# Kernel tuning notes

Hardware: AMD Instinct MI355X
Metric: run time of the kernel (lower is better)

Reference implementation:

```python
import jax, jax.numpy as jnp
import numpy as np

N, E, S = 10000, 100000, 10            # nodes, edges, message-passing steps
NODE_F, EDGE_F, L, H, OUT = 30, 4, 128, 128, 3


def _mlp(h, W0, b0, W1, b1, W2, b2):
    # Linear->ReLU, Linear->ReLU, Linear (build_mlp with num_hidden_layers=2)
    h = jax.nn.relu(h @ W0 + b0)
    h = jax.nn.relu(h @ W1 + b1)
    return h @ W2 + b2


def _ln(h, g, b):
    # torch.nn.LayerNorm over last dim, eps=1e-5, biased variance
    m = h.mean(-1, keepdims=True)
    v = h.var(-1, keepdims=True)
    return (h - m) * jax.lax.rsqrt(v + 1e-5) * g + b


def setup_inputs():
    key = jax.random.key(0)
    ks = iter(jax.random.split(key, 64))

    def w(shape, fan):
        return jax.random.normal(next(ks), shape, dtype=jnp.float32) / np.float32(np.sqrt(fan))

    d = {}
    d["x"] = jax.random.normal(next(ks), (N, NODE_F), dtype=jnp.float32)
    d["ea"] = jax.random.normal(next(ks), (E, EDGE_F), dtype=jnp.float32)
    d["ei"] = jax.random.randint(next(ks), (2, E), 0, N)
    # encoder node ('en') / edge ('ee') MLP+LayerNorm params
    for pre, fin in (("en", NODE_F), ("ee", EDGE_F)):
        d[pre + "W0"] = w((fin, H), fin); d[pre + "b0"] = jnp.zeros((H,), jnp.float32)
        d[pre + "W1"] = w((H, H), H);     d[pre + "b1"] = jnp.zeros((H,), jnp.float32)
        d[pre + "W2"] = w((H, L), H);     d[pre + "b2"] = jnp.zeros((L,), jnp.float32)
        d[pre + "g"] = jnp.ones((L,), jnp.float32); d[pre + "bt"] = jnp.zeros((L,), jnp.float32)
    # processor edge ('pe', in=3L) / node ('pn', in=2L) params, stacked over S steps
    for pre, fin in (("pe", 3 * L), ("pn", 2 * L)):
        d[pre + "W0"] = w((S, fin, H), fin); d[pre + "b0"] = jnp.zeros((S, H), jnp.float32)
        d[pre + "W1"] = w((S, H, H), H);     d[pre + "b1"] = jnp.zeros((S, H), jnp.float32)
        d[pre + "W2"] = w((S, H, L), H);     d[pre + "b2"] = jnp.zeros((S, L), jnp.float32)
        d[pre + "g"] = jnp.ones((S, L), jnp.float32); d[pre + "bt"] = jnp.zeros((S, L), jnp.float32)
    # decoder MLP (no LayerNorm)
    d["dW0"] = w((L, H), L); d["db0"] = jnp.zeros((H,), jnp.float32)
    d["dW1"] = w((H, H), H); d["db1"] = jnp.zeros((H,), jnp.float32)
    d["dW2"] = w((H, OUT), H); d["db2"] = jnp.zeros((OUT,), jnp.float32)
    return d


def reference(x, ea, ei,
              enW0, enb0, enW1, enb1, enW2, enb2, eng, enbt,
              eeW0, eeb0, eeW1, eeb1, eeW2, eeb2, eeg, eebt,
              peW0, peb0, peW1, peb1, peW2, peb2, peg, pebt,
              pnW0, pnb0, pnW1, pnb1, pnW2, pnb2, png, pnbt,
              dW0, db0, dW1, db1, dW2, db2):
    src, dst = ei[0], ei[1]
    # encode (GraphIndependent)
    hx = _ln(_mlp(x, enW0, enb0, enW1, enb1, enW2, enb2), eng, enbt)   # [N, L]
    he = _ln(_mlp(ea, eeW0, eeb0, eeW1, eeb1, eeW2, eeb2), eeg, eebt)  # [E, L]

    # process: S InteractionNetwork steps with residuals
    def step(carry, p):
        cx, ce = carry
        (eW0, eb0, eW1, eb1, eW2, eb2, eg, ebt,
         nW0, nb0, nW1, nb1, nW2, nb2, ng, nbt) = p
        edge_in = jnp.concatenate([cx[src], cx[dst], ce], axis=-1)     # [E, 3L]
        ue = _ln(_mlp(edge_in, eW0, eb0, eW1, eb1, eW2, eb2), eg, ebt)  # [E, L]
        agg = jax.ops.segment_sum(ue, dst, num_segments=N)              # [N, L]
        un = _ln(_mlp(jnp.concatenate([cx, agg], axis=-1), nW0, nb0, nW1, nb1, nW2, nb2), ng, nbt)
        return (cx + un, ce + ue), None

    (hx, he), _ = jax.lax.scan(
        step, (hx, he),
        (peW0, peb0, peW1, peb1, peW2, peb2, peg, pebt,
         pnW0, pnb0, pnW1, pnb1, pnW2, pnb2, png, pnbt))

    # decode
    return _mlp(hx, dW0, db0, dW1, db1, dW2, db2)  # [N, OUT]
```

## Files before the change

### kernel.cpp

```cpp
#include <hip/hip_runtime.h>


#define NN 10000
#define NE 100000
#define STEPS 10
#define NODE_F 30
#define EDGE_F 4
#define L 128
#define AP 132
#define BP 36

#define WS_STRIDE 136
#define AB_STRIDE 136

typedef __bf16 bf16x8 __attribute__((ext_vector_type(8)));
typedef float f32x4 __attribute__((ext_vector_type(4)));

__device__ __forceinline__ unsigned short f2bf(float f) {
  __bf16 b = (__bf16)f;
  return __builtin_bit_cast(unsigned short, b);
}
__device__ __forceinline__ float bf2f(unsigned short u) {
  return __builtin_bit_cast(float, (unsigned)u << 16);
}


__device__ __forceinline__ void stage_W(unsigned short* __restrict__ Ws,
                                        const unsigned short* __restrict__ Wt,
                                        int K, int sec, int tid) {
#pragma unroll
  for (int p = 0; p < 8; ++p) {
    int u = tid + p * 256;
    int n = u >> 4, kk = u & 15;
    uint4 v = *(const uint4*)(Wt + (size_t)n * K + sec * 128 + kk * 8);
    *(uint4*)&Ws[n * WS_STRIDE + kk * 8] = v;
  }
}


__device__ __forceinline__ void init_acc(f32x4 acc[2][4], const float* __restrict__ b,
                                         int wcol, int l16) {
#pragma unroll
  for (int j = 0; j < 4; ++j) {
    float bv = b[wcol + j * 16 + l16];
#pragma unroll
    for (int i = 0; i < 2; ++i) acc[i][j] = f32x4{bv, bv, bv, bv};
  }
}

__device__ __forceinline__ void layer_gbf(const unsigned short* __restrict__ ap0,
                                          const unsigned short* __restrict__ ap1,
                                          const unsigned short* __restrict__ Ws,
                                          f32x4 acc[2][4], int wcol, int l4, int l16) {
#pragma unroll
  for (int kk = 0; kk < 4; ++kk) {
    bf16x8 af[2];
    af[0] = *(const bf16x8*)(ap0 + kk * 32 + l4 * 8);
    af[1] = *(const bf16x8*)(ap1 + kk * 32 + l4 * 8);
#pragma unroll
    for (int j = 0; j < 4; ++j) {
      bf16x8 bv = *(const bf16x8*)&Ws[(wcol + j * 16 + l16) * WS_STRIDE + kk * 32 + l4 * 8];
#pragma unroll
      for (int i = 0; i < 2; ++i)
        acc[i][j] = __builtin_amdgcn_mfma_f32_16x16x32_bf16(af[i], bv, acc[i][j], 0, 0, 0);
    }
  }
}

__device__ __forceinline__ void layer_lds(const unsigned short* __restrict__ Ab,
                                          const unsigned short* __restrict__ Ws,
                                          f32x4 acc[2][4], int wrow, int wcol, int l4, int l16) {
#pragma unroll
  for (int kk = 0; kk < 4; ++kk) {
    bf16x8 af[2];
#pragma unroll
    for (int i = 0; i < 2; ++i)
      af[i] = *(const bf16x8*)&Ab[(wrow + i * 16 + l16) * AB_STRIDE + kk * 32 + l4 * 8];
#pragma unroll
    for (int j = 0; j < 4; ++j) {
      bf16x8 bv = *(const bf16x8*)&Ws[(wcol + j * 16 + l16) * WS_STRIDE + kk * 32 + l4 * 8];
#pragma unroll
      for (int i = 0; i < 2; ++i)
        acc[i][j] = __builtin_amdgcn_mfma_f32_16x16x32_bf16(af[i], bv, acc[i][j], 0, 0, 0);
    }
  }
}

__device__ __forceinline__ void relu_to_Ab(unsigned short* __restrict__ Ab, f32x4 acc[2][4],
                                           int wrow, int wcol, int l4, int l16) {
#pragma unroll
  for (int i = 0; i < 2; ++i)
#pragma unroll
    for (int j = 0; j < 4; ++j)
#pragma unroll
      for (int r = 0; r < 4; ++r) {
        int row = wrow + i * 16 + l4 * 4 + r;
        int col = wcol + j * 16 + l16;
        Ab[row * AB_STRIDE + col] = f2bf(fmaxf(acc[i][j][r], 0.f));
      }
}

__device__ __forceinline__ void ln_partials(const f32x4 acc[2][4], float ps[2][4], float ps2[2][4]) {
#pragma unroll
  for (int i = 0; i < 2; ++i)
#pragma unroll
    for (int r = 0; r < 4; ++r) {
      float s = 0.f, s2 = 0.f;
#pragma unroll
      for (int j = 0; j < 4; ++j) { float v = acc[i][j][r]; s += v; s2 += v * v; }
#pragma unroll
      for (int off = 1; off < 16; off <<= 1) {
        s += __shfl_xor(s, off, 64);
        s2 += __shfl_xor(s2, off, 64);
      }
      ps[i][r] = s; ps2[i][r] = s2;
    }
}


__global__ __launch_bounds__(256) void deg_kernel(const int* __restrict__ ei, int* __restrict__ cnt) {
  int e = blockIdx.x * 256 + threadIdx.x;
  if (e < NE) atomicAdd(&cnt[ei[NE + e]], 1);
}

__global__ __launch_bounds__(256) void scan_kernel(const int* __restrict__ cnt,
                                                   int* __restrict__ off, int* __restrict__ cur) {
  __shared__ int sums[256];
  int t = threadIdx.x;
  int base = t * 40;
  int local = 0;
  for (int i = 0; i < 40; ++i) { int n = base + i; if (n < NN) local += cnt[n]; }
  sums[t] = local;
  __syncthreads();
  int val = local;
  for (int d = 1; d < 256; d <<= 1) {
    int add = (t >= d) ? sums[t - d] : 0;
    __syncthreads();
    sums[t] += add;
    __syncthreads();
  }
  int run = sums[t] - val;
  for (int i = 0; i < 40; ++i) {
    int n = base + i;
    if (n < NN) { off[n] = run; cur[n] = run; run += cnt[n]; }
  }
  if (t == 255) off[NN] = sums[255];
}

__global__ __launch_bounds__(256) void scatter_kernel(const int* __restrict__ ei,
                                                      int* __restrict__ cur, int* __restrict__ eid) {
  int e = blockIdx.x * 256 + threadIdx.x;
  if (e < NE) { int p = atomicAdd(&cur[ei[NE + e]], 1); eid[p] = e; }
}


__global__ __launch_bounds__(256) void edge_step_mfma(
    const unsigned short* __restrict__ hx_bf, unsigned short* __restrict__ he_bf,
    unsigned short* __restrict__ ue_bf,
    const int* __restrict__ ei,
    const unsigned short* __restrict__ W0t, const float* __restrict__ b0,
    const unsigned short* __restrict__ W1t, const float* __restrict__ b1,
    const unsigned short* __restrict__ W2t, const float* __restrict__ b2,
    const float* __restrict__ g, const float* __restrict__ bt) {
  __shared__ __align__(16) unsigned short Ws[128 * WS_STRIDE];
  __shared__ __align__(16) unsigned short Ab[64 * AB_STRIDE];
  __shared__ int sidx[64], didx[64];
  int tid = threadIdx.x;
  int w = tid >> 6, lane = tid & 63;
  int l4 = lane >> 4, l16 = lane & 15;
  int wrow = (w >> 1) * 32, wcol = (w & 1) * 64;
  int e0 = blockIdx.x * 64;
  if (tid < 64) {
    int e = min(e0 + tid, NE - 1);
    sidx[tid] = ei[e];
    didx[tid] = ei[NE + e];
  }
  f32x4 acc[2][4];
  init_acc(acc, b0, wcol, l16);
  __syncthreads();
  for (int sec = 0; sec < 3; ++sec) {
    stage_W(Ws, W0t, 384, sec, tid);
    const unsigned short* ap[2];
#pragma unroll
    for (int i = 0; i < 2; ++i) {
      int r = wrow + i * 16 + l16;
      if (sec == 0)      ap[i] = hx_bf + (size_t)sidx[r] * L;
      else if (sec == 1) ap[i] = hx_bf + (size_t)didx[r] * L;
      else               ap[i] = he_bf + (size_t)min(e0 + r, NE - 1) * L;
    }
    __syncthreads();
    layer_gbf(ap[0], ap[1], Ws, acc, wcol, l4, l16);
    __syncthreads();
  }
  relu_to_Ab(Ab, acc, wrow, wcol, l4, l16);
  stage_W(Ws, W1t, 128, 0, tid);
  init_acc(acc, b1, wcol, l16);
  __syncthreads();
  layer_lds(Ab, Ws, acc, wrow, wcol, l4, l16);
  __syncthreads();
  relu_to_Ab(Ab, acc, wrow, wcol, l4, l16);
  stage_W(Ws, W2t, 128, 0, tid);
  init_acc(acc, b2, wcol, l16);
  __syncthreads();
  layer_lds(Ab, Ws, acc, wrow, wcol, l4, l16);
  float ps[2][4], ps2[2][4];
  ln_partials(acc, ps, ps2);
  __syncthreads();
  float* red = (float*)Ab;
  if (l16 == 0) {
#pragma unroll
    for (int i = 0; i < 2; ++i)
#pragma unroll
      for (int r = 0; r < 4; ++r) {
        int row = wrow + i * 16 + l4 * 4 + r;
        red[(w & 1) * 128 + row * 2 + 0] = ps[i][r];
        red[(w & 1) * 128 + row * 2 + 1] = ps2[i][r];
      }
  }
  __syncthreads();
  float gv[4], btv[4];
#pragma unroll
  for (int j = 0; j < 4; ++j) {
    int col = wcol + j * 16 + l16;
    gv[j] = g[col]; btv[j] = bt[col];
  }
#pragma unroll
  for (int i = 0; i < 2; ++i)
#pragma unroll
    for (int r = 0; r < 4; ++r) {
      int row = wrow + i * 16 + l4 * 4 + r;
      float s  = red[row * 2]     + red[128 + row * 2];
      float s2 = red[row * 2 + 1] + red[128 + row * 2 + 1];
      float m = s * (1.f / 128.f);
      float inv = rsqrtf(s2 * (1.f / 128.f) - m * m + 1e-5f);
      int e = e0 + row;
      if (e < NE) {
        size_t hoff = (size_t)e * L;
#pragma unroll
        for (int j = 0; j < 4; ++j) {
          int col = wcol + j * 16 + l16;
          float u = (acc[i][j][r] - m) * inv * gv[j] + btv[j];
          unsigned short old = he_bf[hoff + col];
          he_bf[hoff + col] = f2bf(bf2f(old) + u);
          ue_bf[hoff + col] = f2bf(u);
        }
      }
    }
}


__global__ __launch_bounds__(256) void node_step_mfma(
    float* __restrict__ hx, unsigned short* __restrict__ hx_bf,
    const unsigned short* __restrict__ ue_bf,
    const int* __restrict__ off, const int* __restrict__ eid,
    const unsigned short* __restrict__ W0t, const float* __restrict__ b0,
    const unsigned short* __restrict__ W1t, const float* __restrict__ b1,
    const unsigned short* __restrict__ W2t, const float* __restrict__ b2,
    const float* __restrict__ g, const float* __restrict__ bt) {
  __shared__ __align__(16) unsigned short Ws[128 * WS_STRIDE];
  __shared__ __align__(16) unsigned short Ab[64 * AB_STRIDE];
  __shared__ __align__(16) unsigned short Ag[64 * AB_STRIDE];
  int tid = threadIdx.x;
  int w = tid >> 6, lane = tid & 63;
  int l4 = lane >> 4, l16 = lane & 15;
  int wrow = (w >> 1) * 32, wcol = (w & 1) * 64;
  int n0 = blockIdx.x * 64;
  {
    int r = tid >> 2;
    int cseg = (tid & 3) * 32;
    int n = n0 + r;
    float a[32];
#pragma unroll
    for (int q = 0; q < 32; ++q) a[q] = 0.f;
    if (n < NN) {
      int p0 = off[n], p1 = off[n + 1];
      for (int p = p0; p < p1; ++p) {
        const unsigned short* row = ue_bf + (size_t)eid[p] * L + cseg;
#pragma unroll
        for (int q = 0; q < 4; ++q) {
          uint4 v = *(const uint4*)(row + q * 8);
          a[q * 8 + 0] += __builtin_bit_cast(float, v.x << 16);
          a[q * 8 + 1] += __builtin_bit_cast(float, v.x & 0xffff0000u);
          a[q * 8 + 2] += __builtin_bit_cast(float, v.y << 16);
          a[q * 8 + 3] += __builtin_bit_cast(float, v.y & 0xffff0000u);
          a[q * 8 + 4] += __builtin_bit_cast(float, v.z << 16);
          a[q * 8 + 5] += __builtin_bit_cast(float, v.z & 0xffff0000u);
          a[q * 8 + 6] += __builtin_bit_cast(float, v.w << 16);
          a[q * 8 + 7] += __builtin_bit_cast(float, v.w & 0xffff0000u);
        }
      }
    }
#pragma unroll
    for (int q = 0; q < 16; ++q) {
      unsigned o = (unsigned)f2bf(a[2 * q]) | ((unsigned)f2bf(a[2 * q + 1]) << 16);
      *(unsigned*)&Ag[r * AB_STRIDE + cseg + 2 * q] = o;
    }
  }
  stage_W(Ws, W0t, 256, 0, tid);
  f32x4 acc[2][4];
  init_acc(acc, b0, wcol, l16);
  __syncthreads();
  {
    const unsigned short* ap[2];
#pragma unroll
    for (int i = 0; i < 2; ++i)
      ap[i] = hx_bf + (size_t)min(n0 + wrow + i * 16 + l16, NN - 1) * L;
    layer_gbf(ap[0], ap[1], Ws, acc, wcol, l4, l16);
  }
  __syncthreads();
  stage_W(Ws, W0t, 256, 1, tid);
  __syncthreads();
  layer_lds(Ag, Ws, acc, wrow, wcol, l4, l16);
  __syncthreads();
  relu_to_Ab(Ab, acc, wrow, wcol, l4, l16);
  stage_W(Ws, W1t, 128, 0, tid);
  init_acc(acc, b1, wcol, l16);
  __syncthreads();
  layer_lds(Ab, Ws, acc, wrow, wcol, l4, l16);
  __syncthreads();
  relu_to_Ab(Ab, acc, wrow, wcol, l4, l16);
  stage_W(Ws, W2t, 128, 0, tid);
  init_acc(acc, b2, wcol, l16);
  __syncthreads();
  layer_lds(Ab, Ws, acc, wrow, wcol, l4, l16);
  float ps[2][4], ps2[2][4];
  ln_partials(acc, ps, ps2);
  __syncthreads();
  float* red = (float*)Ab;
  if (l16 == 0) {
#pragma unroll
    for (int i = 0; i < 2; ++i)
#pragma unroll
      for (int r = 0; r < 4; ++r) {
        int row = wrow + i * 16 + l4 * 4 + r;
        red[(w & 1) * 128 + row * 2 + 0] = ps[i][r];
        red[(w & 1) * 128 + row * 2 + 1] = ps2[i][r];
      }
  }
  __syncthreads();
  float gv[4], btv[4];
#pragma unroll
  for (int j = 0; j < 4; ++j) {
    int col = wcol + j * 16 + l16;
    gv[j] = g[col]; btv[j] = bt[col];
  }
#pragma unroll
  for (int i = 0; i < 2; ++i)
#pragma unroll
    for (int r = 0; r < 4; ++r) {
      int row = wrow + i * 16 + l4 * 4 + r;
      float s  = red[row * 2]     + red[128 + row * 2];
      float s2 = red[row * 2 + 1] + red[128 + row * 2 + 1];
      float m = s * (1.f / 128.f);
      float inv = rsqrtf(s2 * (1.f / 128.f) - m * m + 1e-5f);
      int n = n0 + row;
      if (n < NN) {
#pragma unroll
        for (int j = 0; j < 4; ++j) {
          int col = wcol + j * 16 + l16;
          float un = (acc[i][j][r] - m) * inv * gv[j] + btv[j];
          float nv = hx[(size_t)n * L + col] + un;
          hx[(size_t)n * L + col] = nv;
          hx_bf[(size_t)n * L + col] = f2bf(nv);
        }
      }
    }
}


__global__ __launch_bounds__(256) void enc_edge_mfma(
    const float* __restrict__ ea,
    const float* __restrict__ W0, const float* __restrict__ b0,
    const unsigned short* __restrict__ W1t, const float* __restrict__ b1,
    const unsigned short* __restrict__ W2t, const float* __restrict__ b2,
    const float* __restrict__ g, const float* __restrict__ bt,
    unsigned short* __restrict__ he_bf) {
  __shared__ __align__(16) unsigned short Ws[128 * WS_STRIDE];
  __shared__ __align__(16) unsigned short Ab[64 * AB_STRIDE];
  int tid = threadIdx.x;
  int w = tid >> 6, lane = tid & 63;
  int l4 = lane >> 4, l16 = lane & 15;
  int wrow = (w >> 1) * 32, wcol = (w & 1) * 64;
  int e0 = blockIdx.x * 64;
  {
    int row = tid >> 2, cbase = (tid & 3) * 32;
    int e = min(e0 + row, NE - 1);
    float4 eav = *(const float4*)&ea[(size_t)e * 4];
#pragma unroll
    for (int c = 0; c < 32; ++c) {
      int col = cbase + c;
      float sum = b0[col] + eav.x * W0[col] + eav.y * W0[128 + col] +
                  eav.z * W0[256 + col] + eav.w * W0[384 + col];
      Ab[row * AB_STRIDE + col] = f2bf(fmaxf(sum, 0.f));
    }
  }
  stage_W(Ws, W1t, 128, 0, tid);
  f32x4 acc[2][4];
  init_acc(acc, b1, wcol, l16);
  __syncthreads();
  layer_lds(Ab, Ws, acc, wrow, wcol, l4, l16);
  __syncthreads();
  relu_to_Ab(Ab, acc, wrow, wcol, l4, l16);
  stage_W(Ws, W2t, 128, 0, tid);
  init_acc(acc, b2, wcol, l16);
  __syncthreads();
  layer_lds(Ab, Ws, acc, wrow, wcol, l4, l16);
  float ps[2][4], ps2[2][4];
  ln_partials(acc, ps, ps2);
  __syncthreads();
  float* red = (float*)Ab;
  if (l16 == 0) {
#pragma unroll
    for (int i = 0; i < 2; ++i)
#pragma unroll
      for (int r = 0; r < 4; ++r) {
        int row = wrow + i * 16 + l4 * 4 + r;
        red[(w & 1) * 128 + row * 2 + 0] = ps[i][r];
        red[(w & 1) * 128 + row * 2 + 1] = ps2[i][r];
      }
  }
  __syncthreads();
  float gv[4], btv[4];
#pragma unroll
  for (int j = 0; j < 4; ++j) {
    int col = wcol + j * 16 + l16;
    gv[j] = g[col]; btv[j] = bt[col];
  }
#pragma unroll
  for (int i = 0; i < 2; ++i)
#pragma unroll
    for (int r = 0; r < 4; ++r) {
      int row = wrow + i * 16 + l4 * 4 + r;
      float s  = red[row * 2]     + red[128 + row * 2];
      float s2 = red[row * 2 + 1] + red[128 + row * 2 + 1];
      float m = s * (1.f / 128.f);
      float inv = rsqrtf(s2 * (1.f / 128.f) - m * m + 1e-5f);
      int e = e0 + row;
      if (e < NE) {
#pragma unroll
        for (int j = 0; j < 4; ++j) {
          int col = wcol + j * 16 + l16;
          he_bf[(size_t)e * L + col] = f2bf((acc[i][j][r] - m) * inv * gv[j] + btv[j]);
        }
      }
    }
}


__global__ __launch_bounds__(256) void wprep_kernel(
    const float* __restrict__ W0, const float* __restrict__ W1, const float* __restrict__ W2,
    unsigned short* __restrict__ out, int K0, int steps) {
  int per_step = 128 * (K0 + 256);
  int idx = blockIdx.x * 256 + threadIdx.x;
  if (idx >= steps * per_step) return;
  int s = idx / per_step, r = idx - s * per_step;
  float v;
  if (r < 128 * K0) {
    int n = r / K0, k = r - n * K0;
    v = W0[(size_t)s * K0 * 128 + (size_t)k * 128 + n];
  } else {
    r -= 128 * K0;
    const float* W = (r < 16384) ? W1 : W2;
    r &= 16383;
    int n = r >> 7, k = r & 127;
    v = W[(size_t)s * 16384 + k * 128 + n];
  }
  out[idx] = f2bf(v);
}

__global__ __launch_bounds__(256) void tprep_kernel(
    const float* __restrict__ W1, const float* __restrict__ W2, unsigned short* __restrict__ out) {
  int idx = blockIdx.x * 256 + threadIdx.x;
  const float* W = (idx < 16384) ? W1 : W2;
  int r = idx & 16383;
  int n = r >> 7, k = r & 127;
  out[idx] = f2bf(W[k * 128 + n]);
}


__device__ __forceinline__ void load_B(float* __restrict__ Bs, const float* __restrict__ W,
                                       int K, int k0, int tid) {
#pragma unroll
  for (int p = 0; p < 16; ++p) {
    int idx = tid + p * 256;
    int kk = idx >> 7;
    int c = idx & 127;
    float v = 0.f;
    if (k0 + kk < K) v = W[(size_t)(k0 + kk) * L + c];
    Bs[c * BP + kk] = v;
  }
}

__device__ __forceinline__ void fma32(const float* __restrict__ As, const float* __restrict__ Bs,
                                      float acc[4][8], int ty, int tx, int koff) {
#pragma unroll
  for (int kk = 0; kk < 32; kk += 4) {
    float4 a[4];
    float4 b[8];
#pragma unroll
    for (int i = 0; i < 4; ++i)
      a[i] = *(const float4*)&As[(ty + 16 * i) * AP + koff + kk];
#pragma unroll
    for (int j = 0; j < 8; ++j)
      b[j] = *(const float4*)&Bs[(tx + 16 * j) * BP + kk];
#pragma unroll
    for (int i = 0; i < 4; ++i)
#pragma unroll
      for (int j = 0; j < 8; ++j) {
        acc[i][j] = fmaf(a[i].x, b[j].x, acc[i][j]);
        acc[i][j] = fmaf(a[i].y, b[j].y, acc[i][j]);
        acc[i][j] = fmaf(a[i].z, b[j].z, acc[i][j]);
        acc[i][j] = fmaf(a[i].w, b[j].w, acc[i][j]);
      }
  }
}

__device__ __forceinline__ void init_bias(float acc[4][8], const float* __restrict__ b, int tx) {
#pragma unroll
  for (int j = 0; j < 8; ++j) {
    float bv = b[tx + 16 * j];
#pragma unroll
    for (int i = 0; i < 4; ++i) acc[i][j] = bv;
  }
}

__device__ __forceinline__ void store_relu(float* __restrict__ As, float acc[4][8], int ty, int tx) {
#pragma unroll
  for (int i = 0; i < 4; ++i)
#pragma unroll
    for (int j = 0; j < 8; ++j)
      As[(ty + 16 * i) * AP + tx + 16 * j] = fmaxf(acc[i][j], 0.f);
}

__device__ __forceinline__ void layer_As(const float* __restrict__ As, float* __restrict__ Bs,
                                         const float* __restrict__ W, const float* __restrict__ bias,
                                         int K, float acc[4][8], int tid, int ty, int tx) {
  init_bias(acc, bias, tx);
  int nc = (K + 31) >> 5;
  for (int bc = 0; bc < nc; ++bc) {
    __syncthreads();
    load_B(Bs, W, K, bc * 32, tid);
    __syncthreads();
    fma32(As, Bs, acc, ty, tx, bc * 32);
  }
}

__device__ __forceinline__ void fillA_gather(float* __restrict__ As, const float* __restrict__ base,
                                             const int* __restrict__ ridx, int tid) {
#pragma unroll
  for (int p = 0; p < 8; ++p) {
    int idx = tid + p * 256;
    int r = idx >> 5;
    int c4 = idx & 31;
    float4 v = *(const float4*)&base[(size_t)ridx[r] * L + c4 * 4];
    *(float4*)&As[r * AP + c4 * 4] = v;
  }
}

__device__ __forceinline__ void lnorm(float acc[4][8], const float* __restrict__ g,
                                      const float* __restrict__ bt, int tx) {
  float gv[8], bv[8];
#pragma unroll
  for (int j = 0; j < 8; ++j) { gv[j] = g[tx + 16 * j]; bv[j] = bt[tx + 16 * j]; }
#pragma unroll
  for (int i = 0; i < 4; ++i) {
    float s = 0.f, s2 = 0.f;
#pragma unroll
    for (int j = 0; j < 8; ++j) { s += acc[i][j]; s2 += acc[i][j] * acc[i][j]; }
#pragma unroll
    for (int off = 1; off < 16; off <<= 1) {
      s  += __shfl_xor(s, off, 64);
      s2 += __shfl_xor(s2, off, 64);
    }
    float m = s * (1.f / 128.f);
    float var = s2 * (1.f / 128.f) - m * m;
    float inv = rsqrtf(var + 1e-5f);
#pragma unroll
    for (int j = 0; j < 8; ++j) acc[i][j] = (acc[i][j] - m) * inv * gv[j] + bv[j];
  }
}

__global__ __launch_bounds__(256) void enc_node_kernel(
    const float* __restrict__ x,
    const float* __restrict__ W0, const float* __restrict__ b0,
    const float* __restrict__ W1, const float* __restrict__ b1,
    const float* __restrict__ W2, const float* __restrict__ b2,
    const float* __restrict__ g, const float* __restrict__ bt,
    float* __restrict__ hx, unsigned short* __restrict__ hx_bf) {
  __shared__ float As[64 * AP];
  __shared__ float Bs[128 * BP];
  int tid = threadIdx.x, ty = tid >> 4, tx = tid & 15;
  int n0 = blockIdx.x * 64;
#pragma unroll
  for (int p = 0; p < 8; ++p) {
    int idx = tid + p * 256;
    int r = idx >> 5, c = idx & 31;
    int n = min(n0 + r, NN - 1);
    As[r * AP + c] = (c < NODE_F) ? x[(size_t)n * NODE_F + c] : 0.f;
  }
  float acc[4][8];
  init_bias(acc, b0, tx);
  __syncthreads();
  load_B(Bs, W0, NODE_F, 0, tid);
  __syncthreads();
  fma32(As, Bs, acc, ty, tx, 0);

  __syncthreads(); store_relu(As, acc, ty, tx);
  layer_As(As, Bs, W1, b1, L, acc, tid, ty, tx);
  __syncthreads(); store_relu(As, acc, ty, tx);
  layer_As(As, Bs, W2, b2, L, acc, tid, ty, tx);
  lnorm(acc, g, bt, tx);
#pragma unroll
  for (int i = 0; i < 4; ++i) {
    int n = n0 + ty + 16 * i;
    if (n < NN)
#pragma unroll
      for (int j = 0; j < 8; ++j) {
        float v = acc[i][j];
        hx[(size_t)n * L + tx + 16 * j] = v;
        hx_bf[(size_t)n * L + tx + 16 * j] = f2bf(v);
      }
  }
}

__global__ __launch_bounds__(256) void dec_kernel(
    const float* __restrict__ hx,
    const float* __restrict__ W0, const float* __restrict__ b0,
    const float* __restrict__ W1, const float* __restrict__ b1,
    const float* __restrict__ W2, const float* __restrict__ b2,
    float* __restrict__ out) {
  __shared__ float As[64 * AP];
  __shared__ float Bs[128 * BP];
  __shared__ int nidx[64];
  int tid = threadIdx.x, ty = tid >> 4, tx = tid & 15;
  int n0 = blockIdx.x * 64;
  if (tid < 64) nidx[tid] = min(n0 + tid, NN - 1);
  __syncthreads();
  fillA_gather(As, hx, nidx, tid);
  float acc[4][8];
  layer_As(As, Bs, W0, b0, L, acc, tid, ty, tx);
  __syncthreads(); store_relu(As, acc, ty, tx);
  layer_As(As, Bs, W1, b1, L, acc, tid, ty, tx);
  __syncthreads(); store_relu(As, acc, ty, tx);
  __syncthreads();
  if (tid < 192) {
    int r = tid / 3, o = tid - (tid / 3) * 3;
    int n = n0 + r;
    if (n < NN) {
      float s = b2[o];
#pragma unroll 8
      for (int k = 0; k < L; ++k) s = fmaf(As[r * AP + k], W2[k * 3 + o], s);
      out[(size_t)n * 3 + o] = s;
    }
  }
}


extern "C" void kernel_launch(void* const* d_in, const int* in_sizes, int n_in,
                              void* d_out, int out_size, void* d_ws, size_t ws_size,
                              hipStream_t stream) {
  (void)in_sizes; (void)n_in; (void)out_size; (void)ws_size;
  const float* x    = (const float*)d_in[0];
  const float* ea   = (const float*)d_in[1];
  const int*   ei   = (const int*)d_in[2];
  const float* enW0 = (const float*)d_in[3];  const float* enb0 = (const float*)d_in[4];
  const float* enW1 = (const float*)d_in[5];  const float* enb1 = (const float*)d_in[6];
  const float* enW2 = (const float*)d_in[7];  const float* enb2 = (const float*)d_in[8];
  const float* eng  = (const float*)d_in[9];  const float* enbt = (const float*)d_in[10];
  const float* eeW0 = (const float*)d_in[11]; const float* eeb0 = (const float*)d_in[12];
  const float* eeW1 = (const float*)d_in[13]; const float* eeb1 = (const float*)d_in[14];
  const float* eeW2 = (const float*)d_in[15]; const float* eeb2 = (const float*)d_in[16];
  const float* eeg  = (const float*)d_in[17]; const float* eebt = (const float*)d_in[18];
  const float* peW0 = (const float*)d_in[19]; const float* peb0 = (const float*)d_in[20];
  const float* peW1 = (const float*)d_in[21]; const float* peb1 = (const float*)d_in[22];
  const float* peW2 = (const float*)d_in[23]; const float* peb2 = (const float*)d_in[24];
  const float* peg  = (const float*)d_in[25]; const float* pebt = (const float*)d_in[26];
  const float* pnW0 = (const float*)d_in[27]; const float* pnb0 = (const float*)d_in[28];
  const float* pnW1 = (const float*)d_in[29]; const float* pnb1 = (const float*)d_in[30];
  const float* pnW2 = (const float*)d_in[31]; const float* pnb2 = (const float*)d_in[32];
  const float* png  = (const float*)d_in[33]; const float* pnbt = (const float*)d_in[34];
  const float* dW0  = (const float*)d_in[35]; const float* db0  = (const float*)d_in[36];
  const float* dW1  = (const float*)d_in[37]; const float* db1  = (const float*)d_in[38];
  const float* dW2  = (const float*)d_in[39]; const float* db2  = (const float*)d_in[40];

  const size_t F_HX = (size_t)NN * L, F_HE = (size_t)NE * L;
  const size_t W_PE = 819200, W_PN = 655360, W_EE = 32768;

  float* hx = (float*)d_ws;
  unsigned short* he_bf  = (unsigned short*)(hx + F_HX);
  unsigned short* ue_bf  = he_bf + F_HE;
  unsigned short* hx_bf  = ue_bf + F_HE;
  unsigned short* wt_pe  = hx_bf + F_HX;
  unsigned short* wt_pn  = wt_pe + W_PE;
  unsigned short* wt_ee  = wt_pn + W_PN;
  int* cnt = (int*)(wt_ee + W_EE);
  int* off = cnt + NN;
  int* cur = off + NN + 1;
  int* eid = cur + NN;

  dim3 blk(256);
  int grid_n = (NN + 63) / 64;
  int grid_e = (NE + 63) / 64;

  wprep_kernel<<<(10 * 81920 + 255) / 256, blk, 0, stream>>>(peW0, peW1, peW2, wt_pe, 384, 10);
  wprep_kernel<<<(10 * 65536 + 255) / 256, blk, 0, stream>>>(pnW0, pnW1, pnW2, wt_pn, 256, 10);
  tprep_kernel<<<128, blk, 0, stream>>>(eeW1, eeW2, wt_ee);

  hipMemsetAsync(cnt, 0, (size_t)NN * 4, stream);
  deg_kernel<<<(NE + 255) / 256, blk, 0, stream>>>(ei, cnt);
  scan_kernel<<<1, blk, 0, stream>>>(cnt, off, cur);
  scatter_kernel<<<(NE + 255) / 256, blk, 0, stream>>>(ei, cur, eid);

  enc_node_kernel<<<grid_n, blk, 0, stream>>>(x, enW0, enb0, enW1, enb1, enW2, enb2, eng, enbt, hx, hx_bf);
  enc_edge_mfma<<<grid_e, blk, 0, stream>>>(ea, eeW0, eeb0, wt_ee, eeb1, wt_ee + 16384, eeb2, eeg, eebt, he_bf);

  for (int s = 0; s < STEPS; ++s) {
    const unsigned short* pe = wt_pe + (size_t)s * 81920;
    const unsigned short* pn = wt_pn + (size_t)s * 65536;
    edge_step_mfma<<<grid_e, blk, 0, stream>>>(
        hx_bf, he_bf, ue_bf, ei,
        pe,                 peb0 + (size_t)s * L,
        pe + 49152,         peb1 + (size_t)s * L,
        pe + 49152 + 16384, peb2 + (size_t)s * L,
        peg + (size_t)s * L, pebt + (size_t)s * L);
    node_step_mfma<<<grid_n, blk, 0, stream>>>(
        hx, hx_bf, ue_bf, off, eid,
        pn,                 pnb0 + (size_t)s * L,
        pn + 32768,         pnb1 + (size_t)s * L,
        pn + 32768 + 16384, pnb2 + (size_t)s * L,
        png + (size_t)s * L, pnbt + (size_t)s * L);
  }

  dec_kernel<<<grid_n, blk, 0, stream>>>(hx, dW0, db0, dW1, db1, dW2, db2, (float*)d_out);
}
```

Measured before the change: 947.7 us.

## Process 128 edges per block in edge step to amortize weight staging

The edge-step kernel now handles two 64-edge sub-tiles per block with two accumulator sets. Each staged weight tile in LDS is reused for both sub-tiles, which halves weight staging traffic and block count. Bias, gamma and beta loads are hoisted into registers, and the LayerNorm reduction scratch moves to the Ws buffer. The cost is higher register pressure from doubled accumulators, which may lower occupancy, plus more serialized syncs inside each block.

After: 1.353 ms. 1.43x slower.

```diff
diff --git a/kernel.cpp b/kernel.cpp
--- a/kernel.cpp
+++ b/kernel.cpp
@@ -45,6 +45,15 @@
     float bv = b[wcol + j * 16 + l16];
 #pragma unroll
     for (int i = 0; i < 2; ++i) acc[i][j] = f32x4{bv, bv, bv, bv};
+  }
+}
+
+__device__ __forceinline__ void init_acc_v(f32x4 acc[2][4], const float bv[4]) {
+#pragma unroll
+  for (int j = 0; j < 4; ++j) {
+    f32x4 b = {bv[j], bv[j], bv[j], bv[j]};
+#pragma unroll
+    for (int i = 0; i < 2; ++i) acc[i][j] = b;
   }
 }
 
@@ -164,85 +173,128 @@
     const float* __restrict__ g, const float* __restrict__ bt) {
   __shared__ __align__(16) unsigned short Ws[128 * WS_STRIDE];
   __shared__ __align__(16) unsigned short Ab[64 * AB_STRIDE];
-  __shared__ int sidx[64], didx[64];
+  __shared__ int sidx[128], didx[128];
   int tid = threadIdx.x;
   int w = tid >> 6, lane = tid & 63;
   int l4 = lane >> 4, l16 = lane & 15;
   int wrow = (w >> 1) * 32, wcol = (w & 1) * 64;
-  int e0 = blockIdx.x * 64;
-  if (tid < 64) {
+  int e0 = blockIdx.x * 128;
+  if (tid < 128) {
     int e = min(e0 + tid, NE - 1);
     sidx[tid] = ei[e];
     didx[tid] = ei[NE + e];
   }
-  f32x4 acc[2][4];
-  init_acc(acc, b0, wcol, l16);
+  float bv0[4], bv1[4], bv2[4], gv[4], btv[4];
+#pragma unroll
+  for (int j = 0; j < 4; ++j) {
+    int c = wcol + j * 16 + l16;
+    bv0[j] = b0[c]; bv1[j] = b1[c]; bv2[j] = b2[c]; gv[j] = g[c]; btv[j] = bt[c];
+  }
+  f32x4 acc0[2][4], acc1[2][4];
+  init_acc_v(acc0, bv0);
+  init_acc_v(acc1, bv0);
   __syncthreads();
   for (int sec = 0; sec < 3; ++sec) {
     stage_W(Ws, W0t, 384, sec, tid);
-    const unsigned short* ap[2];
+    const unsigned short* a0[2];
+    const unsigned short* a1[2];
 #pragma unroll
     for (int i = 0; i < 2; ++i) {
       int r = wrow + i * 16 + l16;
-      if (sec == 0)      ap[i] = hx_bf + (size_t)sidx[r] * L;
-      else if (sec == 1) ap[i] = hx_bf + (size_t)didx[r] * L;
-      else               ap[i] = he_bf + (size_t)min(e0 + r, NE - 1) * L;
+      if (sec == 0) {
+        a0[i] = hx_bf + (size_t)sidx[r] * L;
+        a1[i] = hx_bf + (size_t)sidx[64 + r] * L;
+      } else if (sec == 1) {
+        a0[i] = hx_bf + (size_t)didx[r] * L;
+        a1[i] = hx_bf + (size_t)didx[64 + r] * L;
+      } else {
+        a0[i] = he_bf + (size_t)min(e0 + r, NE - 1) * L;
+        a1[i] = he_bf + (size_t)min(e0 + 64 + r, NE - 1) * L;
+      }
     }
     __syncthreads();
-    layer_gbf(ap[0], ap[1], Ws, acc, wcol, l4, l16);
+    layer_gbf(a0[0], a0[1], Ws, acc0, wcol, l4, l16);
+    layer_gbf(a1[0], a1[1], Ws, acc1, wcol, l4, l16);
     __syncthreads();
   }
-  relu_to_Ab(Ab, acc, wrow, wcol, l4, l16);
   stage_W(Ws, W1t, 128, 0, tid);
-  init_acc(acc, b1, wcol, l16);
-  __syncthreads();
-  layer_lds(Ab, Ws, acc, wrow, wcol, l4, l16);
-  __syncthreads();
-  relu_to_Ab(Ab, acc, wrow, wcol, l4, l16);
+  relu_to_Ab(Ab, acc0, wrow, wcol, l4, l16);
+  init_acc_v(acc0, bv1);
+  __syncthreads();
+  layer_lds(Ab, Ws, acc0, wrow, wcol, l4, l16);
+  __syncthreads();
+  relu_to_Ab(Ab, acc1, wrow, wcol, l4, l16);
+  init_acc_v(acc1, bv1);
+  __syncthreads();
+  layer_lds(Ab, Ws, acc1, wrow, wcol, l4, l16);
+  __syncthreads();
   stage_W(Ws, W2t, 128, 0, tid);
-  init_acc(acc, b2, wcol, l16);
-  __syncthreads();
-  layer_lds(Ab, Ws, acc, wrow, wcol, l4, l16);
-  float ps[2][4], ps2[2][4];
-  ln_partials(acc, ps, ps2);
-  __syncthreads();
-  float* red = (float*)Ab;
+  relu_to_Ab(Ab, acc0, wrow, wcol, l4, l16);
+  init_acc_v(acc0, bv2);
+  __syncthreads();
+  layer_lds(Ab, Ws, acc0, wrow, wcol, l4, l16);
+  __syncthreads();
+  relu_to_Ab(Ab, acc1, wrow, wcol, l4, l16);
+  init_acc_v(acc1, bv2);
+  __syncthreads();
+  layer_lds(Ab, Ws, acc1, wrow, wcol, l4, l16);
+  float ps0[2][4], ps20[2][4], ps1[2][4], ps21[2][4];
+  ln_partials(acc0, ps0, ps20);
+  ln_partials(acc1, ps1, ps21);
+  __syncthreads();
+  float* red = (float*)Ws;
   if (l16 == 0) {
 #pragma unroll
     for (int i = 0; i < 2; ++i)
 #pragma unroll
       for (int r = 0; r < 4; ++r) {
         int row = wrow + i * 16 + l4 * 4 + r;
-        red[(w & 1) * 128 + row * 2 + 0] = ps[i][r];
-        red[(w & 1) * 128 + row * 2 + 1] = ps2[i][r];
-      }
-  }
-  __syncthreads();
-  float gv[4], btv[4];
-#pragma unroll
-  for (int j = 0; j < 4; ++j) {
-    int col = wcol + j * 16 + l16;
-    gv[j] = g[col]; btv[j] = bt[col];
-  }
+        red[(w & 1) * 128 + row * 2 + 0] = ps0[i][r];
+        red[(w & 1) * 128 + row * 2 + 1] = ps20[i][r];
+        red[256 + (w & 1) * 128 + row * 2 + 0] = ps1[i][r];
+        red[256 + (w & 1) * 128 + row * 2 + 1] = ps21[i][r];
+      }
+  }
+  __syncthreads();
 #pragma unroll
   for (int i = 0; i < 2; ++i)
 #pragma unroll
     for (int r = 0; r < 4; ++r) {
       int row = wrow + i * 16 + l4 * 4 + r;
-      float s  = red[row * 2]     + red[128 + row * 2];
-      float s2 = red[row * 2 + 1] + red[128 + row * 2 + 1];
-      float m = s * (1.f / 128.f);
-      float inv = rsqrtf(s2 * (1.f / 128.f) - m * m + 1e-5f);
-      int e = e0 + row;
-      if (e < NE) {
-        size_t hoff = (size_t)e * L;
-#pragma unroll
-        for (int j = 0; j < 4; ++j) {
-          int col = wcol + j * 16 + l16;
-          float u = (acc[i][j][r] - m) * inv * gv[j] + btv[j];
-          unsigned short old = he_bf[hoff + col];
-          he_bf[hoff + col] = f2bf(bf2f(old) + u);
-          ue_bf[hoff + col] = f2bf(u);
+      {
+        float s  = red[row * 2]     + red[128 + row * 2];
+        float s2 = red[row * 2 + 1] + red[128 + row * 2 + 1];
+        float m = s * (1.f / 128.f);
+        float inv = rsqrtf(s2 * (1.f / 128.f) - m * m + 1e-5f);
+        int e = e0 + row;
+        if (e < NE) {
+          size_t hoff = (size_t)e * L;
+#pragma unroll
+          for (int j = 0; j < 4; ++j) {
+            int col = wcol + j * 16 + l16;
+            float u = (acc0[i][j][r] - m) * inv * gv[j] + btv[j];
+            unsigned short old = he_bf[hoff + col];
+            he_bf[hoff + col] = f2bf(bf2f(old) + u);
+            ue_bf[hoff + col] = f2bf(u);
+          }
+        }
+      }
+      {
+        float s  = red[256 + row * 2]     + red[256 + 128 + row * 2];
+        float s2 = red[256 + row * 2 + 1] + red[256 + 128 + row * 2 + 1];
+        float m = s * (1.f / 128.f);
+        float inv = rsqrtf(s2 * (1.f / 128.f) - m * m + 1e-5f);
+        int e = e0 + 64 + row;
+        if (e < NE) {
+          size_t hoff = (size_t)e * L;
+#pragma unroll
+          for (int j = 0; j < 4; ++j) {
+            int col = wcol + j * 16 + l16;
+            float u = (acc1[i][j][r] - m) * inv * gv[j] + btv[j];
+            unsigned short old = he_bf[hoff + col];
+            he_bf[hoff + col] = f2bf(bf2f(old) + u);
+            ue_bf[hoff + col] = f2bf(u);
+          }
         }
       }
     }
@@ -408,7 +460,7 @@
   float ps[2][4], ps2[2][4];
   ln_partials(acc, ps, ps2);
   __syncthreads();
-  float* red = (float*)Ab;
+  float* red = (float*)Ws;
   if (l16 == 0) {
 #pragma unroll
     for (int i = 0; i < 2; ++i)
@@ -699,8 +751,9 @@
   int* eid = cur + NN;
 
   dim3 blk(256);
-  int grid_n = (NN + 63) / 64;
-  int grid_e = (NE + 63) / 64;
+  int grid_n    = (NN + 63) / 64;
+  int grid_e64  = (NE + 63) / 64;
+  int grid_e128 = (NE + 127) / 128;
 
   wprep_kernel<<<(10 * 81920 + 255) / 256, blk, 0, stream>>>(peW0, peW1, peW2, wt_pe, 384, 10);
   wprep_kernel<<<(10 * 65536 + 255) / 256, blk, 0, stream>>>(pnW0, pnW1, pnW2, wt_pn, 256, 10);
@@ -712,12 +765,12 @@
   scatter_kernel<<<(NE + 255) / 256, blk, 0, stream>>>(ei, cur, eid);
 
   enc_node_kernel<<<grid_n, blk, 0, stream>>>(x, enW0, enb0, enW1, enb1, enW2, enb2, eng, enbt, hx, hx_bf);
-  enc_edge_mfma<<<grid_e, blk, 0, stream>>>(ea, eeW0, eeb0, wt_ee, eeb1, wt_ee + 16384, eeb2, eeg, eebt, he_bf);
+  enc_edge_mfma<<<grid_e64, blk, 0, stream>>>(ea, eeW0, eeb0, wt_ee, eeb1, wt_ee + 16384, eeb2, eeg, eebt, he_bf);
 
   for (int s = 0; s < STEPS; ++s) {
     const unsigned short* pe = wt_pe + (size_t)s * 81920;
     const unsigned short* pn = wt_pn + (size_t)s * 65536;
-    edge_step_mfma<<<grid_e, blk, 0, stream>>>(
+    edge_step_mfma<<<grid_e128, blk, 0, stream>>>(
         hx_bf, he_bf, ue_bf, ei,
         pe,                 peb0 + (size_t)s * L,
         pe + 49152,         peb1 + (size_t)s * L,
```

## Double-buffer edge-step weight staging in 64-wide K chunks

Applied to the files above, without the earlier changes.

The edge-step kernel now stages weights in 64-column K chunks into two LDS buffers, loading the next chunk while MFMAs consume the current one. This replaces the stage-sync-compute-sync sequence per 128-wide section and cuts barriers that previously serialized loads and math. Bias, gamma and beta loads are hoisted to the kernel start. The LayerNorm reduction scratch moves from Ab to the weight buffer. LDS use stays about the same, with more, smaller stages.

Measured after the change: 1.406 ms. +48.3%, slower.

```diff
diff --git a/kernel.cpp b/kernel.cpp
--- a/kernel.cpp
+++ b/kernel.cpp
@@ -12,6 +12,7 @@
 
 #define WS_STRIDE 136
 #define AB_STRIDE 136
+#define WH_STRIDE 68
 
 typedef __bf16 bf16x8 __attribute__((ext_vector_type(8)));
 typedef float f32x4 __attribute__((ext_vector_type(4)));
@@ -37,6 +38,18 @@
   }
 }
 
+__device__ __forceinline__ void stage64(unsigned short* __restrict__ Ws,
+                                        const unsigned short* __restrict__ Wt,
+                                        int K, int k0, int tid) {
+#pragma unroll
+  for (int p = 0; p < 4; ++p) {
+    int u = tid + p * 256;
+    int n = u >> 3, k8 = u & 7;
+    uint4 v = *(const uint4*)(Wt + (size_t)n * K + k0 + k8 * 8);
+    *(uint4*)&Ws[n * WH_STRIDE + k8 * 8] = v;
+  }
+}
+
 
 __device__ __forceinline__ void init_acc(f32x4 acc[2][4], const float* __restrict__ b,
                                          int wcol, int l16) {
@@ -45,6 +58,53 @@
     float bv = b[wcol + j * 16 + l16];
 #pragma unroll
     for (int i = 0; i < 2; ++i) acc[i][j] = f32x4{bv, bv, bv, bv};
+  }
+}
+
+__device__ __forceinline__ void init_acc_v(f32x4 acc[2][4], const float bv[4]) {
+#pragma unroll
+  for (int j = 0; j < 4; ++j) {
+    f32x4 b = {bv[j], bv[j], bv[j], bv[j]};
+#pragma unroll
+    for (int i = 0; i < 2; ++i) acc[i][j] = b;
+  }
+}
+
+__device__ __forceinline__ void gemm64_g(const unsigned short* __restrict__ ap0,
+                                         const unsigned short* __restrict__ ap1,
+                                         int koff, const unsigned short* __restrict__ Ws,
+                                         f32x4 acc[2][4], int wcol, int l4, int l16) {
+#pragma unroll
+  for (int kk = 0; kk < 2; ++kk) {
+    bf16x8 af[2];
+    af[0] = *(const bf16x8*)(ap0 + koff + kk * 32 + l4 * 8);
+    af[1] = *(const bf16x8*)(ap1 + koff + kk * 32 + l4 * 8);
+#pragma unroll
+    for (int j = 0; j < 4; ++j) {
+      bf16x8 bv = *(const bf16x8*)&Ws[(wcol + j * 16 + l16) * WH_STRIDE + kk * 32 + l4 * 8];
+#pragma unroll
+      for (int i = 0; i < 2; ++i)
+        acc[i][j] = __builtin_amdgcn_mfma_f32_16x16x32_bf16(af[i], bv, acc[i][j], 0, 0, 0);
+    }
+  }
+}
+
+__device__ __forceinline__ void gemm64_l(const unsigned short* __restrict__ Ab, int koff,
+                                         const unsigned short* __restrict__ Ws,
+                                         f32x4 acc[2][4], int wrow, int wcol, int l4, int l16) {
+#pragma unroll
+  for (int kk = 0; kk < 2; ++kk) {
+    bf16x8 af[2];
+#pragma unroll
+    for (int i = 0; i < 2; ++i)
+      af[i] = *(const bf16x8*)&Ab[(wrow + i * 16 + l16) * AB_STRIDE + koff + kk * 32 + l4 * 8];
+#pragma unroll
+    for (int j = 0; j < 4; ++j) {
+      bf16x8 bv = *(const bf16x8*)&Ws[(wcol + j * 16 + l16) * WH_STRIDE + kk * 32 + l4 * 8];
+#pragma unroll
+      for (int i = 0; i < 2; ++i)
+        acc[i][j] = __builtin_amdgcn_mfma_f32_16x16x32_bf16(af[i], bv, acc[i][j], 0, 0, 0);
+    }
   }
 }
 
@@ -162,7 +222,8 @@
     const unsigned short* __restrict__ W1t, const float* __restrict__ b1,
     const unsigned short* __restrict__ W2t, const float* __restrict__ b2,
     const float* __restrict__ g, const float* __restrict__ bt) {
-  __shared__ __align__(16) unsigned short Ws[128 * WS_STRIDE];
+  __shared__ __align__(16) unsigned short WsA[128 * WH_STRIDE];
+  __shared__ __align__(16) unsigned short WsB[128 * WH_STRIDE];
   __shared__ __align__(16) unsigned short Ab[64 * AB_STRIDE];
   __shared__ int sidx[64], didx[64];
   int tid = threadIdx.x;
@@ -175,38 +236,61 @@
     sidx[tid] = ei[e];
     didx[tid] = ei[NE + e];
   }
+  float bv0[4], bv1[4], bv2[4], gv[4], btv[4];
+#pragma unroll
+  for (int j = 0; j < 4; ++j) {
+    int c = wcol + j * 16 + l16;
+    bv0[j] = b0[c]; bv1[j] = b1[c]; bv2[j] = b2[c]; gv[j] = g[c]; btv[j] = bt[c];
+  }
   f32x4 acc[2][4];
-  init_acc(acc, b0, wcol, l16);
-  __syncthreads();
-  for (int sec = 0; sec < 3; ++sec) {
-    stage_W(Ws, W0t, 384, sec, tid);
-    const unsigned short* ap[2];
-#pragma unroll
-    for (int i = 0; i < 2; ++i) {
-      int r = wrow + i * 16 + l16;
-      if (sec == 0)      ap[i] = hx_bf + (size_t)sidx[r] * L;
-      else if (sec == 1) ap[i] = hx_bf + (size_t)didx[r] * L;
-      else               ap[i] = he_bf + (size_t)min(e0 + r, NE - 1) * L;
-    }
-    __syncthreads();
-    layer_gbf(ap[0], ap[1], Ws, acc, wcol, l4, l16);
-    __syncthreads();
-  }
+  init_acc_v(acc, bv0);
+  stage64(WsA, W0t, 384, 0, tid);
+  __syncthreads();
+
+  const unsigned short *asrc[2], *adst[2], *ahe[2];
+#pragma unroll
+  for (int i = 0; i < 2; ++i) {
+    int r = wrow + i * 16 + l16;
+    asrc[i] = hx_bf + (size_t)sidx[r] * L;
+    adst[i] = hx_bf + (size_t)didx[r] * L;
+    ahe[i]  = he_bf + (size_t)min(e0 + r, NE - 1) * L;
+  }
+  stage64(WsB, W0t, 384, 64, tid);
+  gemm64_g(asrc[0], asrc[1], 0, WsA, acc, wcol, l4, l16);
+  __syncthreads();
+  stage64(WsA, W0t, 384, 128, tid);
+  gemm64_g(asrc[0], asrc[1], 64, WsB, acc, wcol, l4, l16);
+  __syncthreads();
+  stage64(WsB, W0t, 384, 192, tid);
+  gemm64_g(adst[0], adst[1], 0, WsA, acc, wcol, l4, l16);
+  __syncthreads();
+  stage64(WsA, W0t, 384, 256, tid);
+  gemm64_g(adst[0], adst[1], 64, WsB, acc, wcol, l4, l16);
+  __syncthreads();
+  stage64(WsB, W0t, 384, 320, tid);
+  gemm64_g(ahe[0], ahe[1], 0, WsA, acc, wcol, l4, l16);
+  __syncthreads();
+  stage64(WsA, W1t, 128, 0, tid);
+  gemm64_g(ahe[0], ahe[1], 64, WsB, acc, wcol, l4, l16);
   relu_to_Ab(Ab, acc, wrow, wcol, l4, l16);
-  stage_W(Ws, W1t, 128, 0, tid);
-  init_acc(acc, b1, wcol, l16);
-  __syncthreads();
-  layer_lds(Ab, Ws, acc, wrow, wcol, l4, l16);
+  init_acc_v(acc, bv1);
+  __syncthreads();
+  stage64(WsB, W1t, 128, 64, tid);
+  gemm64_l(Ab, 0, WsA, acc, wrow, wcol, l4, l16);
+  __syncthreads();
+  stage64(WsA, W2t, 128, 0, tid);
+  gemm64_l(Ab, 64, WsB, acc, wrow, wcol, l4, l16);
   __syncthreads();
   relu_to_Ab(Ab, acc, wrow, wcol, l4, l16);
-  stage_W(Ws, W2t, 128, 0, tid);
-  init_acc(acc, b2, wcol, l16);
-  __syncthreads();
-  layer_lds(Ab, Ws, acc, wrow, wcol, l4, l16);
+  init_acc_v(acc, bv2);
+  __syncthreads();
+  stage64(WsB, W2t, 128, 64, tid);
+  gemm64_l(Ab, 0, WsA, acc, wrow, wcol, l4, l16);
+  __syncthreads();
+  gemm64_l(Ab, 64, WsB, acc, wrow, wcol, l4, l16);
   float ps[2][4], ps2[2][4];
   ln_partials(acc, ps, ps2);
-  __syncthreads();
-  float* red = (float*)Ab;
+  float* red = (float*)WsA;
   if (l16 == 0) {
 #pragma unroll
     for (int i = 0; i < 2; ++i)
@@ -218,12 +302,6 @@
       }
   }
   __syncthreads();
-  float gv[4], btv[4];
-#pragma unroll
-  for (int j = 0; j < 4; ++j) {
-    int col = wcol + j * 16 + l16;
-    gv[j] = g[col]; btv[j] = bt[col];
-  }
 #pragma unroll
   for (int i = 0; i < 2; ++i)
 #pragma unroll
@@ -408,7 +486,7 @@
   float ps[2][4], ps2[2][4];
   ln_partials(acc, ps, ps2);
   __syncthreads();
-  float* red = (float*)Ab;
+  float* red = (float*)Ws;
   if (l16 == 0) {
 #pragma unroll
     for (int i = 0; i < 2; ++i)
```
